# Performance work log

Measured on AMD Instinct MI355X. Metric: run time of the kernel, lower is better.

## Reference

```python
import jax, jax.numpy as jnp
import numpy as np

# MinMaxScaler constants (scaler_X / scaler_fitY), baked in since the original
# reads them from sklearn scaler objects.
F_MIN, F_MAX = 0.0, 1.0          # feature_range for both scalers
X_MIN, X_MAX = 0.0, 500.0        # thickness data range (nm)
Y_MIN, Y_MAX = -2000.0, 2000.0   # stress-thickness data range

D_SETS = 256      # number of datasets (rows of process_c)
SEG_LEN = 65536   # thickness samples per dataset


def stress_equation(params, R, P, T, t):
    """Representative instantaneous-stress law, vectorized over [D, L-1].
    params: [D,4]; R,P,T: [D,1]; t: [D,L-1] film thickness."""
    a, b, c, d = params[:, 0:1], params[:, 1:2], params[:, 2:3], params[:, 3:4]
    return (a * jnp.exp(-t / (jnp.abs(c) + 1e-3))
            + b * jnp.log1p(jnp.abs(t))
            + d * R * P / T)


def setup_inputs() -> dict:
    key = jax.random.key(0)
    k1, k2, k3, k4 = jax.random.split(key, 4)
    x_scaled = jax.random.uniform(k1, (D_SETS * SEG_LEN,), dtype=jnp.float32)
    params = jax.random.normal(k2, (D_SETS, 4), dtype=jnp.float32)
    K0 = jax.random.normal(k3, (D_SETS,), dtype=jnp.float32)
    process_c = jax.random.uniform(k4, (D_SETS, 4), dtype=jnp.float32)
    return {"x_scaled": x_scaled, "params": params, "K0": K0, "process_c": process_c}


def reference(x_scaled, params, K0, process_c):
    D = params.shape[0]
    L = x_scaled.shape[0] // D
    # inverse MinMax transform of thickness, then segment view [D, L]
    t = ((x_scaled - F_MIN) / (F_MAX - F_MIN) * (X_MAX - X_MIN) + X_MIN).reshape(D, L)
    R = process_c[:, 0:1]
    T = process_c[:, 1:2] + 0.1   # keep denominator positive
    P = process_c[:, 2:3]
    # Euler integration: Fit[j+1] = Fit[j] + stress(t[j]) * (t[j+1]-t[j]);  Fit[0] = K0
    dT = t[:, 1:] - t[:, :-1]                                # [D, L-1]
    inc = stress_equation(params, R, P, T, t[:, :-1]) * dT   # [D, L-1]
    fit = K0[:, None] + jnp.concatenate(
        [jnp.zeros((D, 1), dtype=x_scaled.dtype), jnp.cumsum(inc, axis=1)], axis=1)
    # forward MinMax transform of the integrated stress
    out = (fit.reshape(-1) - Y_MIN) / (Y_MAX - Y_MIN) * (F_MAX - F_MIN) + F_MIN
    return out
```

## Files before the change

### kernel.cpp

```cpp
#include <hip/hip_runtime.h>

#define NROWS 256
#define LROW  65536
#define TOT   ((size_t)NROWS * LROW)
#define BLOCK 512
#define VPT   16
#define TILE  (BLOCK * VPT)
#define TPR   (LROW / TILE)
#define NTILE (NROWS * TPR)


__global__ __launch_bounds__(BLOCK)
void stf_scan3(const float* __restrict__ x,
               const float* __restrict__ params,
               const float* __restrict__ k0v,
               const float* __restrict__ procc,
               float* __restrict__ out,
               unsigned long long* __restrict__ state)
{
    const int bid  = blockIdx.x;
    const int d    = bid >> 3;
    const int sub  = bid & 7;
    const int tid  = threadIdx.x;
    const int lane = tid & 63;
    const int wid  = tid >> 6;

    const float pa  = params[d * 4 + 0];
    const float pb  = params[d * 4 + 1];
    const float pcc = params[d * 4 + 2];
    const float pd  = params[d * 4 + 3];
    const float R   = procc[d * 4 + 0];
    const float T   = procc[d * 4 + 1] + 0.1f;
    const float P   = procc[d * 4 + 2];
    const float ec    = -1.44269504f / (fabsf(pcc) + 0.001f);
    const float pb2   = pb * 0.69314718f;
    const float cterm = pd * R * P / T;
    const float k0    = k0v[d];

    const size_t row0 = (size_t)d * LROW;
    const int    g0   = sub * TILE + tid * VPT;
    const float* __restrict__ xp = x + row0 + g0;

    float4 c0 = *(const float4*)(xp + 0);
    float4 c1 = *(const float4*)(xp + 4);
    float4 c2 = *(const float4*)(xp + 8);
    float4 c3 = *(const float4*)(xp + 12);
    float xb = 0.0f;
    if (lane == 63) {
        const size_t gi = row0 + g0 + VPT;
        if (gi < TOT) xb = x[gi];
    }
    float xn = __shfl_down(c0.x, 1);
    if (lane == 63) xn = xb;

    float tv[VPT + 1];
    tv[0]  = c0.x * 500.0f; tv[1]  = c0.y * 500.0f; tv[2]  = c0.z * 500.0f; tv[3]  = c0.w * 500.0f;
    tv[4]  = c1.x * 500.0f; tv[5]  = c1.y * 500.0f; tv[6]  = c1.z * 500.0f; tv[7]  = c1.w * 500.0f;
    tv[8]  = c2.x * 500.0f; tv[9]  = c2.y * 500.0f; tv[10] = c2.z * 500.0f; tv[11] = c2.w * 500.0f;
    tv[12] = c3.x * 500.0f; tv[13] = c3.y * 500.0f; tv[14] = c3.z * 500.0f; tv[15] = c3.w * 500.0f;
    tv[16] = xn * 500.0f;

    const bool isLast = (sub == TPR - 1) && (tid == BLOCK - 1);

    float pref[VPT];
    float run = 0.0f;
    #pragma unroll
    for (int k = 0; k < VPT; ++k) {
        const float t0 = tv[k];
        const float st = pa * exp2f(t0 * ec) + pb2 * __log2f(1.0f + t0) + cterm;
        float inc = st * (tv[k + 1] - t0);
        if (k == VPT - 1) inc = isLast ? 0.0f : inc;
        run += inc;
        pref[k] = run;
    }

    float v = run;
    #pragma unroll
    for (int off = 1; off < 64; off <<= 1) {
        const float other = __shfl_up(v, off);
        if (lane >= off) v += other;
    }
    const float waveExcl = v - run;

    __shared__ float wtot[8];
    __shared__ float wexcl[8];
    __shared__ float s_carry;
    if (lane == 63) wtot[wid] = v;
    __syncthreads();

    if (wid == 0) {
        float wv = (lane < 8) ? wtot[lane] : 0.0f;
        float iv = wv;
        #pragma unroll
        for (int off = 1; off < 8; off <<= 1) {
            const float o = __shfl_up(iv, off);
            if (lane >= off && lane < 8) iv += o;
        }
        if (lane < 8) wexcl[lane] = iv - wv;
        const float total = __shfl(iv, 7);

        if (lane == 0) {
            const unsigned long long packed =
                0x100000000ull | (unsigned long long)__float_as_uint(total);
            __hip_atomic_store(&state[bid], packed,
                               __ATOMIC_RELAXED, __HIP_MEMORY_SCOPE_AGENT);
        }

        float c = 0.0f;
        if (lane < sub) {
            const int pt = bid - 1 - lane;
            unsigned long long w;
            for (;;) {
                w = __hip_atomic_load(&state[pt],
                                      __ATOMIC_RELAXED, __HIP_MEMORY_SCOPE_AGENT);
                if (w >> 32) break;
                __builtin_amdgcn_s_sleep(2);
            }
            c = __uint_as_float((unsigned)w);
        }
        #pragma unroll
        for (int off = 1; off < 8; off <<= 1) c += __shfl_xor(c, off);
        if (lane == 0) s_carry = c;
    }
    __syncthreads();

    const float sc    = 2.5e-4f;
    const float obase = (k0 + s_carry + wexcl[wid] + waveExcl) * sc + 0.5f;

    float4 o0, o1, o2, o3;
    o0.x = obase;
    o0.y = fmaf(pref[0],  sc, obase);
    o0.z = fmaf(pref[1],  sc, obase);
    o0.w = fmaf(pref[2],  sc, obase);
    o1.x = fmaf(pref[3],  sc, obase);
    o1.y = fmaf(pref[4],  sc, obase);
    o1.z = fmaf(pref[5],  sc, obase);
    o1.w = fmaf(pref[6],  sc, obase);
    o2.x = fmaf(pref[7],  sc, obase);
    o2.y = fmaf(pref[8],  sc, obase);
    o2.z = fmaf(pref[9],  sc, obase);
    o2.w = fmaf(pref[10], sc, obase);
    o3.x = fmaf(pref[11], sc, obase);
    o3.y = fmaf(pref[12], sc, obase);
    o3.z = fmaf(pref[13], sc, obase);
    o3.w = fmaf(pref[14], sc, obase);

    float* __restrict__ op = out + row0 + g0;
    *(float4*)(op + 0)  = o0;
    *(float4*)(op + 4)  = o1;
    *(float4*)(op + 8)  = o2;
    *(float4*)(op + 12) = o3;
}

extern "C" void kernel_launch(void* const* d_in, const int* in_sizes, int n_in,
                              void* d_out, int out_size, void* d_ws, size_t ws_size,
                              hipStream_t stream) {
    const float* x      = (const float*)d_in[0];
    const float* params = (const float*)d_in[1];
    const float* K0     = (const float*)d_in[2];
    const float* procc  = (const float*)d_in[3];
    float* out = (float*)d_out;
    unsigned long long* state = (unsigned long long*)d_ws;

    hipMemsetAsync(d_ws, 0, NTILE * sizeof(unsigned long long), stream);
    stf_scan3<<<NTILE, BLOCK, 0, stream>>>(x, params, K0, procc, out, state);
}
```

Baseline: 130.8 us.

## Stage tile through swizzled LDS for coalesced global loads and stores

After: 121.8 us. -6.8%, faster.

```diff
diff --git a/kernel.cpp b/kernel.cpp
--- a/kernel.cpp
+++ b/kernel.cpp
@@ -10,8 +10,10 @@
 #define NTILE (NROWS * TPR)
 
 
+__device__ __forceinline__ int sw(int e) { return e ^ (((e >> 4) & 3) << 2); }
+
 __global__ __launch_bounds__(BLOCK)
-void stf_scan3(const float* __restrict__ x,
+void stf_scan5(const float* __restrict__ x,
                const float* __restrict__ params,
                const float* __restrict__ k0v,
                const float* __restrict__ procc,
@@ -25,6 +27,12 @@
     const int lane = tid & 63;
     const int wid  = tid >> 6;
 
+    __shared__ float tile[TILE];
+    __shared__ float baseArr[BLOCK];
+    __shared__ float wtot[8];
+    __shared__ float wexcl[8];
+    __shared__ float s_carry;
+
     const float pa  = params[d * 4 + 0];
     const float pb  = params[d * 4 + 1];
     const float pcc = params[d * 4 + 2];
@@ -37,54 +45,63 @@
     const float cterm = pd * R * P / T;
     const float k0    = k0v[d];
 
-    const size_t row0 = (size_t)d * LROW;
-    const int    g0   = sub * TILE + tid * VPT;
-    const float* __restrict__ xp = x + row0 + g0;
+    const size_t tbase = (size_t)d * LROW + (size_t)sub * TILE;
 
-    float4 c0 = *(const float4*)(xp + 0);
-    float4 c1 = *(const float4*)(xp + 4);
-    float4 c2 = *(const float4*)(xp + 8);
-    float4 c3 = *(const float4*)(xp + 12);
-    float xb = 0.0f;
-    if (lane == 63) {
-        const size_t gi = row0 + g0 + VPT;
-        if (gi < TOT) xb = x[gi];
+    const float* __restrict__ xp = x + tbase + tid * 4;
+    float4 L0 = *(const float4*)(xp + 0 * 2048);
+    float4 L1 = *(const float4*)(xp + 1 * 2048);
+    float4 L2 = *(const float4*)(xp + 2 * 2048);
+    float4 L3 = *(const float4*)(xp + 3 * 2048);
+    float bxg = 0.0f;
+    if (tid == BLOCK - 1) {
+        const size_t gi = tbase + TILE;
+        if (gi < TOT) bxg = x[gi];
     }
-    float xn = __shfl_down(c0.x, 1);
-    if (lane == 63) xn = xb;
 
-    float tv[VPT + 1];
-    tv[0]  = c0.x * 500.0f; tv[1]  = c0.y * 500.0f; tv[2]  = c0.z * 500.0f; tv[3]  = c0.w * 500.0f;
-    tv[4]  = c1.x * 500.0f; tv[5]  = c1.y * 500.0f; tv[6]  = c1.z * 500.0f; tv[7]  = c1.w * 500.0f;
-    tv[8]  = c2.x * 500.0f; tv[9]  = c2.y * 500.0f; tv[10] = c2.z * 500.0f; tv[11] = c2.w * 500.0f;
-    tv[12] = c3.x * 500.0f; tv[13] = c3.y * 500.0f; tv[14] = c3.z * 500.0f; tv[15] = c3.w * 500.0f;
-    tv[16] = xn * 500.0f;
+    *(float4*)&tile[sw(0 * 2048 + tid * 4)] = L0;
+    *(float4*)&tile[sw(1 * 2048 + tid * 4)] = L1;
+    *(float4*)&tile[sw(2 * 2048 + tid * 4)] = L2;
+    *(float4*)&tile[sw(3 * 2048 + tid * 4)] = L3;
+    __syncthreads();
 
-    const bool isLast = (sub == TPR - 1) && (tid == BLOCK - 1);
+    const float bnd = (tid < BLOCK - 1) ? tile[sw((tid + 1) * VPT)] : bxg;
+    __syncthreads();
 
-    float pref[VPT];
-    float run = 0.0f;
+    const int eb = tid * VPT;
+    float4 cur = *(const float4*)&tile[sw(eb)];
+    float run = 0.0f, sprev = 0.0f;
     #pragma unroll
-    for (int k = 0; k < VPT; ++k) {
-        const float t0 = tv[k];
-        const float st = pa * exp2f(t0 * ec) + pb2 * __log2f(1.0f + t0) + cterm;
-        float inc = st * (tv[k + 1] - t0);
-        if (k == VPT - 1) inc = isLast ? 0.0f : inc;
-        run += inc;
-        pref[k] = run;
+    for (int g = 0; g < 4; ++g) {
+        float4 nxt;
+        if (g < 3) nxt = *(const float4*)&tile[sw(eb + 4 * (g + 1))];
+        else       nxt = make_float4(bnd, 0.0f, 0.0f, 0.0f);
+
+        const float ta = cur.x * 500.0f, tb = cur.y * 500.0f;
+        const float tc = cur.z * 500.0f, td = cur.w * 500.0f;
+        const float te = nxt.x * 500.0f;
+
+        float4 s4;
+        s4.x = sprev;
+        run += (pa * exp2f(ta * ec) + pb2 * __log2f(1.0f + ta) + cterm) * (tb - ta);
+        s4.y = run;
+        run += (pa * exp2f(tb * ec) + pb2 * __log2f(1.0f + tb) + cterm) * (tc - tb);
+        s4.z = run;
+        run += (pa * exp2f(tc * ec) + pb2 * __log2f(1.0f + tc) + cterm) * (td - tc);
+        s4.w = run;
+        run += (pa * exp2f(td * ec) + pb2 * __log2f(1.0f + td) + cterm) * (te - td);
+        sprev = run;
+
+        *(float4*)&tile[sw(eb + 4 * g)] = s4;
+        cur = nxt;
     }
 
     float v = run;
     #pragma unroll
     for (int off = 1; off < 64; off <<= 1) {
-        const float other = __shfl_up(v, off);
-        if (lane >= off) v += other;
+        const float o = __shfl_up(v, off);
+        if (lane >= off) v += o;
     }
     const float waveExcl = v - run;
-
-    __shared__ float wtot[8];
-    __shared__ float wexcl[8];
-    __shared__ float s_carry;
     if (lane == 63) wtot[wid] = v;
     __syncthreads();
 
@@ -105,7 +122,6 @@
             __hip_atomic_store(&state[bid], packed,
                                __ATOMIC_RELAXED, __HIP_MEMORY_SCOPE_AGENT);
         }
-
         float c = 0.0f;
         if (lane < sub) {
             const int pt = bid - 1 - lane;
@@ -124,32 +140,22 @@
     }
     __syncthreads();
 
-    const float sc    = 2.5e-4f;
-    const float obase = (k0 + s_carry + wexcl[wid] + waveExcl) * sc + 0.5f;
+    baseArr[tid] = k0 + s_carry + wexcl[wid] + waveExcl;
+    __syncthreads();
 
-    float4 o0, o1, o2, o3;
-    o0.x = obase;
-    o0.y = fmaf(pref[0],  sc, obase);
-    o0.z = fmaf(pref[1],  sc, obase);
-    o0.w = fmaf(pref[2],  sc, obase);
-    o1.x = fmaf(pref[3],  sc, obase);
-    o1.y = fmaf(pref[4],  sc, obase);
-    o1.z = fmaf(pref[5],  sc, obase);
-    o1.w = fmaf(pref[6],  sc, obase);
-    o2.x = fmaf(pref[7],  sc, obase);
-    o2.y = fmaf(pref[8],  sc, obase);
-    o2.z = fmaf(pref[9],  sc, obase);
-    o2.w = fmaf(pref[10], sc, obase);
-    o3.x = fmaf(pref[11], sc, obase);
-    o3.y = fmaf(pref[12], sc, obase);
-    o3.z = fmaf(pref[13], sc, obase);
-    o3.w = fmaf(pref[14], sc, obase);
-
-    float* __restrict__ op = out + row0 + g0;
-    *(float4*)(op + 0)  = o0;
-    *(float4*)(op + 4)  = o1;
-    *(float4*)(op + 8)  = o2;
-    *(float4*)(op + 12) = o3;
+    const float scl = 2.5e-4f;
+    float* __restrict__ op = out + tbase + tid * 4;
+    #pragma unroll
+    for (int r = 0; r < 4; ++r) {
+        const float4 sv = *(const float4*)&tile[sw(r * 2048 + tid * 4)];
+        const float b = baseArr[r * 128 + (tid >> 2)];
+        float4 o;
+        o.x = (sv.x + b) * scl + 0.5f;
+        o.y = (sv.y + b) * scl + 0.5f;
+        o.z = (sv.z + b) * scl + 0.5f;
+        o.w = (sv.w + b) * scl + 0.5f;
+        *(float4*)(op + r * 2048) = o;
+    }
 }
 
 extern "C" void kernel_launch(void* const* d_in, const int* in_sizes, int n_in,
@@ -163,5 +169,5 @@
     unsigned long long* state = (unsigned long long*)d_ws;
 
     hipMemsetAsync(d_ws, 0, NTILE * sizeof(unsigned long long), stream);
-    stf_scan3<<<NTILE, BLOCK, 0, stream>>>(x, params, K0, procc, out, state);
+    stf_scan5<<<NTILE, BLOCK, 0, stream>>>(x, params, K0, procc, out, state);
 }
```
